# Kernel optimization log

Measured on AMD Instinct MI355X. Metric: run time of the kernel, lower is better.

Reference implementation:

```python
import jax, jax.numpy as jnp
import numpy as np
from jax import lax

T = 8  # hardcoded temporal length in the torch module

def _dwconv_t(z, w, b):
    # z: (N, C, T, 1); w: (C, 1, k, 1) depthwise; 'same' padding along T
    k = w.shape[2]
    p = (k - 1) // 2
    out = lax.conv_general_dilated(
        z, w, window_strides=(1, 1), padding=[(p, p), (0, 0)],
        feature_group_count=z.shape[1],
        dimension_numbers=('NCHW', 'OIHW', 'NCHW'))
    return out + b[None, :, None, None]


def setup_inputs() -> dict:
    key = jax.random.key(0)
    ks = jax.random.split(key, 13)
    C, IC, H, W, B = 1024, 512, 14, 14, 16
    s = lambda k, shp, scale: jax.random.normal(k, shp, dtype=jnp.float32) * scale
    return {
        'x':   s(ks[0], (B * T, C, H, W), 1.0),
        'w1':  s(ks[1], (IC, C, 1, 1), 0.03),
        'b1':  s(ks[2], (IC,), 0.02),
        'wb1': s(ks[3], (IC, 1, 1, 1), 0.3),
        'bb1': s(ks[4], (IC,), 0.02),
        'wb2': s(ks[5], (IC, 1, 3, 1), 0.3),
        'bb2': s(ks[6], (IC,), 0.02),
        'wb3': s(ks[7], (IC, 1, 5, 1), 0.3),
        'bb3': s(ks[8], (IC,), 0.02),
        'wb4': s(ks[9], (IC, 1, 7, 1), 0.3),
        'bb4': s(ks[10], (IC,), 0.02),
        'w2':  s(ks[11], (C, IC, 1, 1), 0.03),
        'b2':  s(ks[12], (C,), 0.02),
    }


def reference(x, w1, b1, wb1, bb1, wb2, bb2, wb3, bb3, wb4, bb4, w2, b2):
    BT, C, H, W = x.shape
    B = BT // T
    IC = w1.shape[0]
    # conv1: 1x1 pointwise conv == channel GEMM
    y = jnp.einsum('nchw,oc->nohw', x, w1[:, :, 0, 0]) + b1[None, :, None, None]
    # (B*T, IC, H, W) -> (B, T, IC, H, W) -> (B, H, W, IC, T) -> (B*H*W, IC, T, 1)
    z = y.reshape(B, T, IC, H, W).transpose(0, 3, 4, 2, 1).reshape(B * H * W, IC, T, 1)
    out = (_dwconv_t(z, wb1, bb1) + _dwconv_t(z, wb2, bb2)
           + _dwconv_t(z, wb3, bb3) + _dwconv_t(z, wb4, bb4))
    # (B*H*W, IC, T, 1) -> (B, H, W, IC, T) -> (B, T, IC, H, W) -> (B*T, IC, H, W)
    out = out.reshape(B, H, W, IC, T).transpose(0, 4, 3, 1, 2).reshape(BT, IC, H, W)
    # conv2: 1x1 pointwise conv back to C channels
    out = jnp.einsum('nihw,oi->nohw', out, w2[:, :, 0, 0]) + b2[None, :, None, None]
    return x + out
```

## Files before the change

kernel.cpp:

```cpp
#include <hip/hip_runtime.h>
#include <hip/hip_bf16.h>

typedef short short8 __attribute__((ext_vector_type(8)));
typedef float f32x4 __attribute__((ext_vector_type(4)));
typedef unsigned int uint;

#define CB   16
#define TT   8
#define CIN  1024
#define ICH  512
#define HWS  196
#define NPB  1568
#define NF   25088

static __device__ __forceinline__ unsigned short f2bf(float f) {
  __hip_bfloat16 h = __float2bfloat16(f); unsigned short u; __builtin_memcpy(&u, &h, 2); return u;
}

static __device__ __forceinline__ void stage16(const void* g, void* l) {
  __builtin_amdgcn_global_load_lds(
      (const __attribute__((address_space(1))) unsigned int*)(unsigned long long)g,
      (__attribute__((address_space(3))) unsigned int*)(unsigned int)(unsigned long long)l,
      16, 0, 0);
}

__global__ void k_prep_w(const float* __restrict__ w1, const float* __restrict__ w2,
    const float* __restrict__ wb1, const float* __restrict__ bb1,
    const float* __restrict__ wb2, const float* __restrict__ bb2,
    const float* __restrict__ wb3, const float* __restrict__ bb3,
    const float* __restrict__ wb4, const float* __restrict__ bb4,
    __hip_bfloat16* __restrict__ w1b, __hip_bfloat16* __restrict__ w2b,
    float* __restrict__ weff, float* __restrict__ beff) {
  int g = blockIdx.x * 256 + threadIdx.x;
  int idx4 = g * 4;
  if (idx4 < CIN * ICH) {
    float4 a = *(const float4*)(w1 + idx4);
    ushort4 pa = {f2bf(a.x), f2bf(a.y), f2bf(a.z), f2bf(a.w)};
    *(ushort4*)((unsigned short*)w1b + idx4) = pa;
    float4 b = *(const float4*)(w2 + idx4);
    ushort4 pb = {f2bf(b.x), f2bf(b.y), f2bf(b.z), f2bf(b.w)};
    *(ushort4*)((unsigned short*)w2b + idx4) = pb;
  }
  if (g < ICH) {
    float e[7];
#pragma unroll
    for (int u = 0; u < 7; u++) e[u] = wb4[g * 7 + u];
#pragma unroll
    for (int u = 0; u < 5; u++) e[u + 1] += wb3[g * 5 + u];
#pragma unroll
    for (int u = 0; u < 3; u++) e[u + 2] += wb2[g * 3 + u];
    e[3] += wb1[g];
#pragma unroll
    for (int u = 0; u < 7; u++) weff[g * 8 + u] = e[u];
    weff[g * 8 + 7] = 0.f;
    beff[g] = bb1[g] + bb2[g] + bb3[g] + bb4[g];
  }
}

__global__ __launch_bounds__(448) void k_prep_x(const float* __restrict__ x,
                                                __hip_bfloat16* __restrict__ xbT) {
  __shared__ unsigned short tile[196 * 128];
  int xcd = blockIdx.x & 7, i = blockIdx.x >> 3;
  int id = xcd * 128 + i;
  int bt = id >> 3, cr = id & 7;
  int c0 = cr * 128;
  int b = bt >> 3, t = bt & 7;
  const float* src = x + ((size_t)bt * CIN + c0) * HWS;
  int tid = threadIdx.x;
#pragma unroll
  for (int it = 0; it < 14; it++) {
    int idx = it * 448 + tid;
    f32x4 v = *(const f32x4*)(src + (size_t)idx * 4);
    int c = idx / 49, hwq = idx - c * 49;
#pragma unroll
    for (int j = 0; j < 4; j++) {
      int hw = hwq * 4 + j;
      int slot = (c >> 3) ^ ((hw + (hw >> 2)) & 15);
      tile[hw * 128 + slot * 8 + (c & 7)] = f2bf(v[j]);
    }
  }
  __syncthreads();
  __hip_bfloat16* dstb = xbT + ((size_t)b * NPB + (size_t)t) * CIN + c0;
#pragma unroll
  for (int it = 0; it < 7; it++) {
    int idx = it * 448 + tid;
    int hw = idx >> 4, co = idx & 15;
    int slot = co ^ ((hw + (hw >> 2)) & 15);
    uint4 val = *(const uint4*)&tile[hw * 128 + slot * 8];
    *(uint4*)(dstb + (size_t)(hw * 8) * CIN + co * 8) = val;
  }
}

template <int KD>
static __device__ __forceinline__ void gemm_core16(
    const __hip_bfloat16* __restrict__ Ar,
    const __hip_bfloat16* __restrict__ Br,
    __hip_bfloat16* As, __hip_bfloat16* Bs, f32x4 (&acc)[4][4]) {
  constexpr int NT = KD / 64;
  const int tid = threadIdx.x;
  const int lane = tid & 63, w = tid >> 6;
  const int wm = w >> 2, wn = w & 3;
  const int ln = lane & 15, lm = lane >> 4;
  const int srow = lane >> 3;
  const int schk = (lane & 7) ^ srow;
  const __hip_bfloat16* aS = Ar + (size_t)(w * 8 + srow) * KD + schk * 8;
  const __hip_bfloat16* bS = Br + (size_t)(w * 8 + srow) * KD + schk * 8;
  __hip_bfloat16* aD = As + (w * 8) * 64;
  __hip_bfloat16* bD = Bs + (w * 8) * 64;
  const int ck0 = ((lm) ^ (ln & 7)) * 8;
  const int ck1 = ((4 + lm) ^ (ln & 7)) * 8;
  const int rab = (wm * 16 + ln) * 64;
  const int rbb = (wn * 64 + ln) * 64;

#define STG(src, dst, h, kt, buf) \
  stage16(src + (size_t)((h) * 128) * KD + (kt) * 64, dst + (buf) * 16384 + ((h) * 128) * 64)

  STG(bS, bD, 0, 0, 0); STG(bS, bD, 1, 0, 0);
  STG(aS, aD, 0, 0, 0); STG(aS, aD, 1, 0, 0);

  short8 af0, af1, bfA[4], bfB[4];
  for (int t = 0; t < NT; t++) {
    const int buf = t & 1, nb = buf ^ 1;
    const bool has = (t + 1 < NT);
    const __hip_bfloat16* Ab = As + buf * 16384;
    const __hip_bfloat16* Bb = Bs + buf * 16384;
    if (has) STG(bS, bD, 0, t + 1, nb);
    if (has) asm volatile("s_waitcnt vmcnt(2)" ::: "memory");
    else     asm volatile("s_waitcnt vmcnt(1)" ::: "memory");
    asm volatile("s_barrier" ::: "memory");
    af0 = *(const short8*)&Ab[rab + ck0];
    af1 = *(const short8*)&Ab[rab + 4096 + ck0];
#pragma unroll
    for (int nf = 0; nf < 4; nf++) bfA[nf] = *(const short8*)&Bb[rbb + nf * 1024 + ck0];
    asm volatile("s_waitcnt lgkmcnt(0)" ::: "memory");
    __builtin_amdgcn_sched_barrier(0);
    __builtin_amdgcn_s_setprio(1);
#pragma unroll
    for (int nf = 0; nf < 4; nf++) {
      acc[0][nf] = __builtin_amdgcn_mfma_f32_16x16x32_bf16(af0, bfA[nf], acc[0][nf], 0, 0, 0);
      acc[1][nf] = __builtin_amdgcn_mfma_f32_16x16x32_bf16(af1, bfA[nf], acc[1][nf], 0, 0, 0);
    }
    __builtin_amdgcn_s_setprio(0);
    if (has) STG(bS, bD, 1, t + 1, nb);
    af0 = *(const short8*)&Ab[rab + ck1];
    af1 = *(const short8*)&Ab[rab + 4096 + ck1];
#pragma unroll
    for (int nf = 0; nf < 4; nf++) bfB[nf] = *(const short8*)&Bb[rbb + nf * 1024 + ck1];
    asm volatile("s_waitcnt lgkmcnt(0)" ::: "memory");
    __builtin_amdgcn_sched_barrier(0);
    __builtin_amdgcn_s_setprio(1);
#pragma unroll
    for (int nf = 0; nf < 4; nf++) {
      acc[0][nf] = __builtin_amdgcn_mfma_f32_16x16x32_bf16(af0, bfB[nf], acc[0][nf], 0, 0, 0);
      acc[1][nf] = __builtin_amdgcn_mfma_f32_16x16x32_bf16(af1, bfB[nf], acc[1][nf], 0, 0, 0);
    }
    __builtin_amdgcn_s_setprio(0);
    if (has) STG(aS, aD, 0, t + 1, nb);
    if (has) asm volatile("s_waitcnt vmcnt(3)" ::: "memory");
    else     asm volatile("s_waitcnt vmcnt(0)" ::: "memory");
    asm volatile("s_barrier" ::: "memory");
    af0 = *(const short8*)&Ab[rab + 2 * 4096 + ck0];
    af1 = *(const short8*)&Ab[rab + 3 * 4096 + ck0];
    asm volatile("s_waitcnt lgkmcnt(0)" ::: "memory");
    __builtin_amdgcn_sched_barrier(0);
    __builtin_amdgcn_s_setprio(1);
#pragma unroll
    for (int nf = 0; nf < 4; nf++) {
      acc[2][nf] = __builtin_amdgcn_mfma_f32_16x16x32_bf16(af0, bfA[nf], acc[2][nf], 0, 0, 0);
      acc[3][nf] = __builtin_amdgcn_mfma_f32_16x16x32_bf16(af1, bfA[nf], acc[3][nf], 0, 0, 0);
    }
    __builtin_amdgcn_s_setprio(0);
    if (has) STG(aS, aD, 1, t + 1, nb);
    af0 = *(const short8*)&Ab[rab + 2 * 4096 + ck1];
    af1 = *(const short8*)&Ab[rab + 3 * 4096 + ck1];
    asm volatile("s_waitcnt lgkmcnt(0)" ::: "memory");
    __builtin_amdgcn_sched_barrier(0);
    asm volatile("s_barrier" ::: "memory");
    __builtin_amdgcn_s_setprio(1);
#pragma unroll
    for (int nf = 0; nf < 4; nf++) {
      acc[2][nf] = __builtin_amdgcn_mfma_f32_16x16x32_bf16(af0, bfB[nf], acc[2][nf], 0, 0, 0);
      acc[3][nf] = __builtin_amdgcn_mfma_f32_16x16x32_bf16(af1, bfB[nf], acc[3][nf], 0, 0, 0);
    }
    __builtin_amdgcn_s_setprio(0);
  }
#undef STG
}

__global__ __launch_bounds__(1024, 4) void k_gemm1(const __hip_bfloat16* __restrict__ xbT,
                                                   const __hip_bfloat16* __restrict__ w1b,
                                                   const float* __restrict__ b1,
                                                   const float* __restrict__ weff,
                                                   const float* __restrict__ beff,
                                                   __hip_bfloat16* __restrict__ dwT) {
  __shared__ __hip_bfloat16 As[2 * 256 * 64];
  __shared__ __hip_bfloat16 Bs[2 * 256 * 64];
  int xcd = blockIdx.x & 7, i = blockIdx.x >> 3;
  int id = (xcd < 4 ? xcd * 25 : 100 + (xcd - 4) * 24) + i;
  int rt = id >> 1, ot = id & 1;
  int n0 = rt * 256, o0 = ot * 256;
  f32x4 acc[4][4];
#pragma unroll
  for (int a = 0; a < 4; a++)
#pragma unroll
    for (int c = 0; c < 4; c++) acc[a][c] = (f32x4){0.f, 0.f, 0.f, 0.f};
  gemm_core16<1024>(xbT + (size_t)n0 * CIN, w1b + (size_t)o0 * CIN, As, Bs, acc);

  int tid = threadIdx.x, lane = tid & 63, w = tid >> 6;
  int wm = w >> 2, wn = w & 3, ln = lane & 15, lm = lane >> 4;
  bool hiT = (lm & 1);
#pragma unroll
  for (int nf = 0; nf < 4; nf++) {
    int o = o0 + wn * 64 + nf * 16 + ln;
    float e[7];
#pragma unroll
    for (int u = 0; u < 7; u++) e[u] = weff[o * 8 + u];
    float be = beff[o];
    float bo = b1[o];
#pragma unroll
    for (int mf = 0; mf < 4; mf++) {
      float av[4], pv[4];
#pragma unroll
      for (int j = 0; j < 4; j++) av[j] = acc[mf][nf][j] + bo;
#pragma unroll
      for (int j = 0; j < 4; j++) pv[j] = __shfl_xor(av[j], 16, 64);
      float ov[4];
      if (hiT) {
#pragma unroll
        for (int j = 0; j < 4; j++) {
          float s = be;
#pragma unroll
          for (int u = 0; u < 7; u++) {
            int ss = 4 + j + u - 3;
            if (ss >= 0 && ss < 8) s += e[u] * (ss < 4 ? pv[ss] : av[ss - 4]);
          }
          ov[j] = s;
        }
      } else {
#pragma unroll
        for (int j = 0; j < 4; j++) {
          float s = be;
#pragma unroll
          for (int u = 0; u < 7; u++) {
            int ss = j + u - 3;
            if (ss >= 0 && ss < 8) s += e[u] * (ss < 4 ? av[ss] : pv[ss - 4]);
          }
          ov[j] = s;
        }
      }
      int grow = n0 + mf * 64 + wm * 16 + ((lm >> 1) & 1) * 8;
      int gidx = grow >> 3;
      int gb = gidx / HWS, ghw = gidx - gb * HWS;
      int tb = hiT ? 4 : 0;
#pragma unroll
      for (int j = 0; j < 4; j++) {
        size_t rr = (size_t)gb * NPB + (size_t)(tb + j) * HWS + ghw;
        dwT[rr * ICH + o] = __float2bfloat16(ov[j]);
      }
    }
  }
}

__global__ __launch_bounds__(1024, 4) void k_gemm2(const __hip_bfloat16* __restrict__ dwT,
                                                   const __hip_bfloat16* __restrict__ w2b,
                                                   const float* __restrict__ b2,
                                                   const float* __restrict__ xres,
                                                   float* __restrict__ out) {
  __shared__ __align__(16) char smem[131072];
  __hip_bfloat16* As = (__hip_bfloat16*)smem;
  __hip_bfloat16* Bs = (__hip_bfloat16*)(smem + 65536);
  int id = (blockIdx.x & 7) * 49 + (blockIdx.x >> 3);
  int nt = id >> 2, mt = id & 3;
  int n0 = nt * 256, m0 = mt * 256;
  f32x4 acc[4][4];
#pragma unroll
  for (int a = 0; a < 4; a++)
#pragma unroll
    for (int c = 0; c < 4; c++) acc[a][c] = (f32x4){0.f, 0.f, 0.f, 0.f};
  gemm_core16<512>(w2b + (size_t)m0 * ICH, dwT + (size_t)n0 * ICH, As, Bs, acc);

  int tid = threadIdx.x, lane = tid & 63, w = tid >> 6;
  int wm = w >> 2, wn = w & 3, ln = lane & 15, lm = lane >> 4;
  float* arr = (float*)smem;
  int fc = tid & 63, fr = tid >> 6;
  int n2 = n0 + fc * 4;
  int bb = n2 / NPB, r = n2 - bb * NPB;
  int t2 = r / HWS, hw = r - t2 * HWS;
  size_t base4 = ((size_t)((bb * TT + t2) * CIN)) * HWS + hw;
#pragma unroll
  for (int p = 0; p < 4; p++) {
    __syncthreads();
#pragma unroll
    for (int nf = 0; nf < 4; nf++)
#pragma unroll
      for (int j = 0; j < 4; j++)
        arr[(wm * 16 + lm * 4 + j) * 260 + wn * 64 + nf * 16 + ln] = acc[p][nf][j];
    __syncthreads();
#pragma unroll
    for (int it = 0; it < 4; it++) {
      int o2l = it * 16 + fr;
      f32x4 v = *(const f32x4*)&arr[o2l * 260 + fc * 4];
      int o2 = m0 + p * 64 + o2l;
      float bo = b2[o2];
      size_t a = base4 + (size_t)o2 * HWS;
      float4 xr = *(const float4*)(xres + a);
      float4 ov = make_float4(v[0] + bo + xr.x, v[1] + bo + xr.y,
                              v[2] + bo + xr.z, v[3] + bo + xr.w);
      *(float4*)(out + a) = ov;
    }
  }
}

extern "C" void kernel_launch(void* const* d_in, const int* in_sizes, int n_in,
                              void* d_out, int out_size, void* d_ws, size_t ws_size,
                              hipStream_t stream) {
  const float* x   = (const float*)d_in[0];
  const float* w1  = (const float*)d_in[1];
  const float* b1  = (const float*)d_in[2];
  const float* wb1 = (const float*)d_in[3];
  const float* bb1 = (const float*)d_in[4];
  const float* wb2 = (const float*)d_in[5];
  const float* bb2 = (const float*)d_in[6];
  const float* wb3 = (const float*)d_in[7];
  const float* bb3 = (const float*)d_in[8];
  const float* wb4 = (const float*)d_in[9];
  const float* bb4 = (const float*)d_in[10];
  const float* w2  = (const float*)d_in[11];
  const float* b2  = (const float*)d_in[12];
  float* out = (float*)d_out;

  __hip_bfloat16* xbT = (__hip_bfloat16*)d_out;

  char* ws = (char*)d_ws;
  __hip_bfloat16* dwT = (__hip_bfloat16*)ws;
  __hip_bfloat16* w1b = (__hip_bfloat16*)(ws + 25690112);
  __hip_bfloat16* w2b = (__hip_bfloat16*)(ws + 25690112 + 1048576);
  float* weff = (float*)(ws + 25690112 + 2097152);
  float* beff = weff + 4096;

  k_prep_w<<<512, 256, 0, stream>>>(
      w1, w2, wb1, bb1, wb2, bb2, wb3, bb3, wb4, bb4, w1b, w2b, weff, beff);
  k_prep_x<<<1024, 448, 0, stream>>>(x, xbT);
  k_gemm1<<<196, 1024, 0, stream>>>(xbT, w1b, b1, weff, beff, dwT);
  k_gemm2<<<392, 1024, 0, stream>>>(dwT, w2b, b2, x, out);
}
```

Baseline: 117.4 us.

## Fuse x fp32-to-bf16 transpose into GEMM1 A-tile loading

Removes the separate k_prep_x kernel that converted x to a transposed bf16 buffer. GEMM1 now loads fp32 x directly with vector loads into registers, converts to bf16 and writes swizzled rows into LDS inside the pipelined K loop, while B still streams via global_load_lds. This avoids writing and rereading an intermediate bf16 copy of x and one kernel launch. In exchange the per-thread A loads are strided and need register staging plus more LDS store instructions in the main loop, which may stall the MFMA pipeline.

```diff
diff --git a/kernel.cpp b/kernel.cpp
--- a/kernel.cpp
+++ b/kernel.cpp
@@ -57,37 +57,210 @@
   }
 }
 
-__global__ __launch_bounds__(448) void k_prep_x(const float* __restrict__ x,
-                                                __hip_bfloat16* __restrict__ xbT) {
-  __shared__ unsigned short tile[196 * 128];
+__global__ __launch_bounds__(1024, 4) void k_gemm1(const float* __restrict__ x,
+                                                   const __hip_bfloat16* __restrict__ w1b,
+                                                   const float* __restrict__ b1,
+                                                   const float* __restrict__ weff,
+                                                   const float* __restrict__ beff,
+                                                   __hip_bfloat16* __restrict__ dwT) {
+  __shared__ __hip_bfloat16 As[2 * 256 * 64];
+  __shared__ __hip_bfloat16 Bs[2 * 256 * 64];
   int xcd = blockIdx.x & 7, i = blockIdx.x >> 3;
-  int id = xcd * 128 + i;
-  int bt = id >> 3, cr = id & 7;
-  int c0 = cr * 128;
-  int b = bt >> 3, t = bt & 7;
-  const float* src = x + ((size_t)bt * CIN + c0) * HWS;
-  int tid = threadIdx.x;
-#pragma unroll
-  for (int it = 0; it < 14; it++) {
-    int idx = it * 448 + tid;
-    f32x4 v = *(const f32x4*)(src + (size_t)idx * 4);
-    int c = idx / 49, hwq = idx - c * 49;
-#pragma unroll
-    for (int j = 0; j < 4; j++) {
-      int hw = hwq * 4 + j;
-      int slot = (c >> 3) ^ ((hw + (hw >> 2)) & 15);
-      tile[hw * 128 + slot * 8 + (c & 7)] = f2bf(v[j]);
-    }
-  }
-  __syncthreads();
-  __hip_bfloat16* dstb = xbT + ((size_t)b * NPB + (size_t)t) * CIN + c0;
-#pragma unroll
-  for (int it = 0; it < 7; it++) {
-    int idx = it * 448 + tid;
-    int hw = idx >> 4, co = idx & 15;
-    int slot = co ^ ((hw + (hw >> 2)) & 15);
-    uint4 val = *(const uint4*)&tile[hw * 128 + slot * 8];
-    *(uint4*)(dstb + (size_t)(hw * 8) * CIN + co * 8) = val;
+  int id = (xcd < 4 ? xcd * 25 : 100 + (xcd - 4) * 24) + i;
+  int rt = id >> 1, ot = id & 1;
+  int gidx0 = rt * 32, o0 = ot * 256;
+  const int tid = threadIdx.x;
+  const int lane = tid & 63, w = tid >> 6;
+  const int wm = w >> 2, wn = w & 3;
+  const int ln = lane & 15, lm = lane >> 4;
+
+  const int hwq = lane & 7;
+  const int ccA = (w & 7) * 8 + (lane >> 3);
+  const int tA0 = (w >> 3);
+  int g4 = gidx0 + hwq * 4;
+  int b4 = g4 / HWS;
+  int hw4 = g4 - b4 * HWS;
+  const float* xbase = x + ((size_t)(b4 * TT + tA0) * CIN + ccA) * HWS + hw4;
+  const int wslot = (ccA >> 3);
+  unsigned short* AsW = (unsigned short*)As;
+
+  const int srow = lane >> 3;
+  const int schk = (lane & 7) ^ srow;
+  const __hip_bfloat16* bS = w1b + (size_t)(o0 + w * 8 + srow) * CIN + schk * 8;
+  __hip_bfloat16* bD = Bs + (w * 8) * 64;
+#define STGB(h, kt, buf) \
+  stage16(bS + (size_t)((h) * 128) * CIN + (kt) * 64, bD + (buf) * 16384 + ((h) * 128) * 64)
+
+  const int ckB0 = ((lm) ^ (ln & 7)) * 8;
+  const int rbb = (wn * 64 + ln) * 64;
+  int raA[4];
+#pragma unroll
+  for (int mf = 0; mf < 4; mf++) {
+    int row = mf * 64 + wm * 16 + ln;
+    int ch = lm ^ (row & 7) ^ ((row >> 5) & 7);
+    raA[mf] = row * 64 + ch * 8;
+  }
+
+  f32x4 acc[4][4];
+#pragma unroll
+  for (int a = 0; a < 4; a++)
+#pragma unroll
+    for (int c = 0; c < 4; c++) acc[a][c] = (f32x4){0.f, 0.f, 0.f, 0.f};
+
+  f32x4 av0 = *(const f32x4*)(xbase);
+  f32x4 av1 = *(const f32x4*)(xbase + 401408);
+  f32x4 av2 = *(const f32x4*)(xbase + 802816);
+  f32x4 av3 = *(const f32x4*)(xbase + 1204224);
+  STGB(0, 0, 0); STGB(1, 0, 0);
+  asm volatile("s_waitcnt vmcnt(2)" ::: "memory");
+  {
+#pragma unroll
+    for (int it = 0; it < 4; it++) {
+      f32x4 v = (it == 0) ? av0 : (it == 1) ? av1 : (it == 2) ? av2 : av3;
+      int tt = tA0 + it * 2;
+      int sb = (wslot ^ tt ^ hwq) * 8 + (ccA & 7);
+#pragma unroll
+      for (int j = 0; j < 4; j++)
+        AsW[(hwq * 32 + j * 8 + tt) * 64 + sb] = f2bf(v[j]);
+    }
+  }
+  asm volatile("s_waitcnt lgkmcnt(0)" ::: "memory");
+
+  short8 af0, af1, bfA[4], bfB[4];
+  for (int t = 0; t < 16; t++) {
+    const int buf = t & 1, nb = buf ^ 1;
+    const bool has = (t < 15);
+    const __hip_bfloat16* Ab = As + buf * 16384;
+    const __hip_bfloat16* Bb = Bs + buf * 16384;
+    if (has) {
+      const float* pk = xbase + (size_t)(t + 1) * 12544;
+      av0 = *(const f32x4*)pk;
+      av1 = *(const f32x4*)(pk + 401408);
+      av2 = *(const f32x4*)(pk + 802816);
+      av3 = *(const f32x4*)(pk + 1204224);
+      STGB(0, t + 1, nb);
+      asm volatile("s_waitcnt vmcnt(5)" ::: "memory");
+    } else {
+      asm volatile("s_waitcnt vmcnt(0)" ::: "memory");
+    }
+    asm volatile("s_barrier" ::: "memory");
+    af0 = *(const short8*)&Ab[raA[0]];
+    af1 = *(const short8*)&Ab[raA[1]];
+#pragma unroll
+    for (int nf = 0; nf < 4; nf++) bfA[nf] = *(const short8*)&Bb[rbb + nf * 1024 + ckB0];
+    asm volatile("s_waitcnt lgkmcnt(0)" ::: "memory");
+    __builtin_amdgcn_sched_barrier(0);
+    __builtin_amdgcn_s_setprio(1);
+#pragma unroll
+    for (int nf = 0; nf < 4; nf++) {
+      acc[0][nf] = __builtin_amdgcn_mfma_f32_16x16x32_bf16(af0, bfA[nf], acc[0][nf], 0, 0, 0);
+      acc[1][nf] = __builtin_amdgcn_mfma_f32_16x16x32_bf16(af1, bfA[nf], acc[1][nf], 0, 0, 0);
+    }
+    __builtin_amdgcn_s_setprio(0);
+    if (has) STGB(1, t + 1, nb);
+    af0 = *(const short8*)&Ab[raA[0] ^ 32];
+    af1 = *(const short8*)&Ab[raA[1] ^ 32];
+#pragma unroll
+    for (int nf = 0; nf < 4; nf++) bfB[nf] = *(const short8*)&Bb[rbb + nf * 1024 + (ckB0 ^ 32)];
+    asm volatile("s_waitcnt lgkmcnt(0)" ::: "memory");
+    __builtin_amdgcn_sched_barrier(0);
+    __builtin_amdgcn_s_setprio(1);
+#pragma unroll
+    for (int nf = 0; nf < 4; nf++) {
+      acc[0][nf] = __builtin_amdgcn_mfma_f32_16x16x32_bf16(af0, bfB[nf], acc[0][nf], 0, 0, 0);
+      acc[1][nf] = __builtin_amdgcn_mfma_f32_16x16x32_bf16(af1, bfB[nf], acc[1][nf], 0, 0, 0);
+    }
+    __builtin_amdgcn_s_setprio(0);
+    af0 = *(const short8*)&Ab[raA[2]];
+    af1 = *(const short8*)&Ab[raA[3]];
+    asm volatile("s_waitcnt lgkmcnt(0)" ::: "memory");
+    __builtin_amdgcn_sched_barrier(0);
+    __builtin_amdgcn_s_setprio(1);
+#pragma unroll
+    for (int nf = 0; nf < 4; nf++) {
+      acc[2][nf] = __builtin_amdgcn_mfma_f32_16x16x32_bf16(af0, bfA[nf], acc[2][nf], 0, 0, 0);
+      acc[3][nf] = __builtin_amdgcn_mfma_f32_16x16x32_bf16(af1, bfA[nf], acc[3][nf], 0, 0, 0);
+    }
+    __builtin_amdgcn_s_setprio(0);
+    if (has) {
+      asm volatile("s_waitcnt vmcnt(2)" ::: "memory");
+      unsigned short* dst = AsW + nb * 16384;
+#pragma unroll
+      for (int it = 0; it < 4; it++) {
+        f32x4 v = (it == 0) ? av0 : (it == 1) ? av1 : (it == 2) ? av2 : av3;
+        int tt = tA0 + it * 2;
+        int sb = (wslot ^ tt ^ hwq) * 8 + (ccA & 7);
+#pragma unroll
+        for (int j = 0; j < 4; j++)
+          dst[(hwq * 32 + j * 8 + tt) * 64 + sb] = f2bf(v[j]);
+      }
+    }
+    af0 = *(const short8*)&Ab[raA[2] ^ 32];
+    af1 = *(const short8*)&Ab[raA[3] ^ 32];
+    asm volatile("s_waitcnt lgkmcnt(0)" ::: "memory");
+    __builtin_amdgcn_sched_barrier(0);
+    if (has) asm volatile("s_barrier" ::: "memory");
+    __builtin_amdgcn_s_setprio(1);
+#pragma unroll
+    for (int nf = 0; nf < 4; nf++) {
+      acc[2][nf] = __builtin_amdgcn_mfma_f32_16x16x32_bf16(af0, bfB[nf], acc[2][nf], 0, 0, 0);
+      acc[3][nf] = __builtin_amdgcn_mfma_f32_16x16x32_bf16(af1, bfB[nf], acc[3][nf], 0, 0, 0);
+    }
+    __builtin_amdgcn_s_setprio(0);
+  }
+#undef STGB
+
+  int n0 = rt * 256;
+  bool hiT = (lm & 1);
+#pragma unroll
+  for (int nf = 0; nf < 4; nf++) {
+    int o = o0 + wn * 64 + nf * 16 + ln;
+    float e[7];
+#pragma unroll
+    for (int u = 0; u < 7; u++) e[u] = weff[o * 8 + u];
+    float be = beff[o];
+    float bo = b1[o];
+#pragma unroll
+    for (int mf = 0; mf < 4; mf++) {
+      float av[4], pv[4];
+#pragma unroll
+      for (int j = 0; j < 4; j++) av[j] = acc[mf][nf][j] + bo;
+#pragma unroll
+      for (int j = 0; j < 4; j++) pv[j] = __shfl_xor(av[j], 16, 64);
+      float ov[4];
+      if (hiT) {
+#pragma unroll
+        for (int j = 0; j < 4; j++) {
+          float s = be;
+#pragma unroll
+          for (int u = 0; u < 7; u++) {
+            int ss = 4 + j + u - 3;
+            if (ss >= 0 && ss < 8) s += e[u] * (ss < 4 ? pv[ss] : av[ss - 4]);
+          }
+          ov[j] = s;
+        }
+      } else {
+#pragma unroll
+        for (int j = 0; j < 4; j++) {
+          float s = be;
+#pragma unroll
+          for (int u = 0; u < 7; u++) {
+            int ss = j + u - 3;
+            if (ss >= 0 && ss < 8) s += e[u] * (ss < 4 ? av[ss] : pv[ss - 4]);
+          }
+          ov[j] = s;
+        }
+      }
+      int grow = n0 + mf * 64 + wm * 16 + ((lm >> 1) & 1) * 8;
+      int gidx = grow >> 3;
+      int gb = gidx / HWS, ghw = gidx - gb * HWS;
+      int tb = hiT ? 4 : 0;
+#pragma unroll
+      for (int j = 0; j < 4; j++) {
+        size_t rr = (size_t)gb * NPB + (size_t)(tb + j) * HWS + ghw;
+        dwT[rr * ICH + o] = __float2bfloat16(ov[j]);
+      }
+    }
   }
 }
 
@@ -187,80 +360,6 @@
 #undef STG
 }
 
-__global__ __launch_bounds__(1024, 4) void k_gemm1(const __hip_bfloat16* __restrict__ xbT,
-                                                   const __hip_bfloat16* __restrict__ w1b,
-                                                   const float* __restrict__ b1,
-                                                   const float* __restrict__ weff,
-                                                   const float* __restrict__ beff,
-                                                   __hip_bfloat16* __restrict__ dwT) {
-  __shared__ __hip_bfloat16 As[2 * 256 * 64];
-  __shared__ __hip_bfloat16 Bs[2 * 256 * 64];
-  int xcd = blockIdx.x & 7, i = blockIdx.x >> 3;
-  int id = (xcd < 4 ? xcd * 25 : 100 + (xcd - 4) * 24) + i;
-  int rt = id >> 1, ot = id & 1;
-  int n0 = rt * 256, o0 = ot * 256;
-  f32x4 acc[4][4];
-#pragma unroll
-  for (int a = 0; a < 4; a++)
-#pragma unroll
-    for (int c = 0; c < 4; c++) acc[a][c] = (f32x4){0.f, 0.f, 0.f, 0.f};
-  gemm_core16<1024>(xbT + (size_t)n0 * CIN, w1b + (size_t)o0 * CIN, As, Bs, acc);
-
-  int tid = threadIdx.x, lane = tid & 63, w = tid >> 6;
-  int wm = w >> 2, wn = w & 3, ln = lane & 15, lm = lane >> 4;
-  bool hiT = (lm & 1);
-#pragma unroll
-  for (int nf = 0; nf < 4; nf++) {
-    int o = o0 + wn * 64 + nf * 16 + ln;
-    float e[7];
-#pragma unroll
-    for (int u = 0; u < 7; u++) e[u] = weff[o * 8 + u];
-    float be = beff[o];
-    float bo = b1[o];
-#pragma unroll
-    for (int mf = 0; mf < 4; mf++) {
-      float av[4], pv[4];
-#pragma unroll
-      for (int j = 0; j < 4; j++) av[j] = acc[mf][nf][j] + bo;
-#pragma unroll
-      for (int j = 0; j < 4; j++) pv[j] = __shfl_xor(av[j], 16, 64);
-      float ov[4];
-      if (hiT) {
-#pragma unroll
-        for (int j = 0; j < 4; j++) {
-          float s = be;
-#pragma unroll
-          for (int u = 0; u < 7; u++) {
-            int ss = 4 + j + u - 3;
-            if (ss >= 0 && ss < 8) s += e[u] * (ss < 4 ? pv[ss] : av[ss - 4]);
-          }
-          ov[j] = s;
-        }
-      } else {
-#pragma unroll
-        for (int j = 0; j < 4; j++) {
-          float s = be;
-#pragma unroll
-          for (int u = 0; u < 7; u++) {
-            int ss = j + u - 3;
-            if (ss >= 0 && ss < 8) s += e[u] * (ss < 4 ? av[ss] : pv[ss - 4]);
-          }
-          ov[j] = s;
-        }
-      }
-      int grow = n0 + mf * 64 + wm * 16 + ((lm >> 1) & 1) * 8;
-      int gidx = grow >> 3;
-      int gb = gidx / HWS, ghw = gidx - gb * HWS;
-      int tb = hiT ? 4 : 0;
-#pragma unroll
-      for (int j = 0; j < 4; j++) {
-        size_t rr = (size_t)gb * NPB + (size_t)(tb + j) * HWS + ghw;
-        dwT[rr * ICH + o] = __float2bfloat16(ov[j]);
-      }
-    }
-  }
-}
-
 __global__ __launch_bounds__(1024, 4) void k_gemm2(const __hip_bfloat16* __restrict__ dwT,
                                                    const __hip_bfloat16* __restrict__ w2b,
                                                    const float* __restrict__ b2,
@@ -329,8 +428,6 @@
   const float* b2  = (const float*)d_in[12];
   float* out = (float*)d_out;
 
-  __hip_bfloat16* xbT = (__hip_bfloat16*)d_out;
-
   char* ws = (char*)d_ws;
   __hip_bfloat16* dwT = (__hip_bfloat16*)ws;
   __hip_bfloat16* w1b = (__hip_bfloat16*)(ws + 25690112);
@@ -340,7 +437,6 @@
 
   k_prep_w<<<512, 256, 0, stream>>>(
       w1, w2, wb1, bb1, wb2, bb2, wb3, bb3, wb4, bb4, w1b, w2b, weff, beff);
-  k_prep_x<<<1024, 448, 0, stream>>>(x, xbT);
-  k_gemm1<<<196, 1024, 0, stream>>>(xbT, w1b, b1, weff, beff, dwT);
+  k_gemm1<<<196, 1024, 0, stream>>>(x, w1b, b1, weff, beff, dwT);
   k_gemm2<<<392, 1024, 0, stream>>>(dwT, w2b, b2, x, out);
 }
```

Result: slower. 162.6 us (+38.5%).
